# Optimization experiments

Hardware: AMD Instinct MI355X
Metric: run time of the kernel (lower is better)

The kernel has to match this reference:

```python
import jax, jax.numpy as jnp
import numpy as np
from jax import lax

N_GROUPS, TOP_K, CALIB_SCALE = 4, 3, 2.0


def setup_inputs() -> dict:
    key = jax.random.key(0)
    ks = jax.random.split(key, 32)
    d = {}
    d['x'] = jax.random.normal(ks[0], (64, 64, 8192), jnp.float32)
    d['conv_weight'] = jax.random.normal(ks[1], (64, 64, 3), jnp.float32) * 0.05
    d['bias'] = jax.random.normal(ks[2], (64,), jnp.float32) * 0.05
    d['grads'] = jax.random.normal(ks[3], (12288,), jnp.float32) * 0.01
    d['q_ema'] = jax.random.normal(ks[4], (4416,), jnp.float32) * 0.1
    d['ctrl_w'] = jax.random.normal(ks[5], (64, 192), jnp.float32) * 0.07
    d['ctrl_b'] = jnp.zeros((64,), jnp.float32)
    d['gp_w'] = jax.random.normal(ks[6], (64, 65), jnp.float32) * 0.1
    d['gp_b'] = jnp.zeros((64,), jnp.float32)
    d['gt_w'] = jax.random.normal(ks[7], (64, 64), jnp.float32) * 0.1
    d['gt_b'] = jnp.zeros((64,), jnp.float32)
    d['ln_g'] = jnp.ones((64,), jnp.float32)
    d['ln_b'] = jnp.zeros((64,), jnp.float32)
    d['ccin_w'] = jax.random.normal(ks[8], (64, 64), jnp.float32) * 0.05
    d['ccin_b'] = jnp.zeros((64,), jnp.float32)
    d['ck_w'] = jax.random.normal(ks[9], (3, 64), jnp.float32) * 0.05
    d['ck_b'] = jnp.zeros((3,), jnp.float32)
    d['cb_w'] = jax.random.normal(ks[10], (1, 64), jnp.float32) * 0.05
    d['cb_b'] = jnp.zeros((1,), jnp.float32)
    d['cf_w'] = jax.random.normal(ks[11], (1, 64), jnp.float32) * 0.05
    d['cf_b'] = jnp.zeros((1,), jnp.float32)
    d['tau_w'] = jax.random.normal(ks[12], (1, 64), jnp.float32) * 0.1
    d['tau_b'] = jnp.zeros((1,), jnp.float32)
    W = jax.random.normal(ks[13], (4, 1104, 32), jnp.float32)
    d['mem_W'] = W / jnp.linalg.norm(W, axis=1, keepdims=True)  # column-normalized codebook
    d['temp_logit'] = jnp.zeros((4,), jnp.float32)
    return d


def reference(x, conv_weight, bias, grads, q_ema, ctrl_w, ctrl_b, gp_w, gp_b,
              gt_w, gt_b, ln_g, ln_b, ccin_w, ccin_b, ck_w, ck_b, cb_w, cb_b,
              cf_w, cf_b, tau_w, tau_b, mem_W, temp_logit):
    C_out, C_in, K = conv_weight.shape
    cpg = C_out // N_GROUPS
    cin_tot, k_tot = C_out * C_in, C_out * K
    shift = 0.0  # shift_magnitude

    # --- controller: grads -> calibration query q ---
    g = grads.reshape(C_out, C_in * K)
    h = jax.nn.silu(g @ ctrl_w.T + ctrl_b)
    gn = jnp.linalg.norm(g, axis=-1, keepdims=True)
    z = jax.nn.sigmoid(jnp.concatenate([h, gn], -1) @ gp_w.T + gp_b)
    h_t = jax.nn.silu(h @ gt_w.T + gt_b)
    hm = (1.0 - z) * h + z * h_t
    mu = hm.mean(-1, keepdims=True)
    var = ((hm - mu) ** 2).mean(-1, keepdims=True)
    h = ln_g * (hm - mu) / jnp.sqrt(var + 1e-5) + ln_b

    w_cin = jnp.tanh(h @ ccin_w.T + ccin_b) * CALIB_SCALE   # [C_out, C_in]
    w_k = jnp.tanh(h @ ck_w.T + ck_b) * CALIB_SCALE         # [C_out, K]
    b_r = jnp.tanh(h @ cb_w.T + cb_b)[:, 0] * CALIB_SCALE   # [C_out]
    f_r = jnp.tanh(h @ cf_w.T + cf_b)[:, 0] * CALIB_SCALE   # [C_out]
    tau = jax.nn.sigmoid(h @ tau_w.T + tau_b).mean() * 0.5 + 0.5

    q = jnp.concatenate([w_cin.reshape(-1), w_k.reshape(-1), b_r, f_r])
    q = 0.7 * q + 0.3 * lax.stop_gradient(q_ema)

    # --- channel-grouped codebook retrieval (trigger path) ---
    qd = lax.stop_gradient(q)
    q_groups = jnp.concatenate([
        qd[:cin_tot].reshape(N_GROUPS, cpg * C_in),
        qd[cin_tot:cin_tot + k_tot].reshape(N_GROUPS, cpg * K),
        qd[cin_tot + k_tot:cin_tot + k_tot + C_out].reshape(N_GROUPS, cpg),
        qd[cin_tot + k_tot + C_out:].reshape(N_GROUPS, cpg)], axis=1)  # [G, gq]
    temp = (jax.nn.sigmoid(temp_logit) * 0.6 + 0.2) / (1.0 + shift)     # [G]
    att = jnp.einsum('gd,gdm->gm', q_groups, mem_W)
    att = jax.nn.softmax(att / (temp[:, None] + 1e-8), axis=1)
    v, idx = lax.top_k(att, TOP_K)                                      # [G, k]
    gath = jnp.take_along_axis(mem_W, idx[:, None, :], axis=2)          # [G, gq, k]
    retrieved = (gath * v[:, None, :]).sum(-1)                          # [G, gq]

    s0, s1, s2 = cpg * C_in, cpg * (C_in + K), cpg * (C_in + K + 1)
    retrieved_global = jnp.concatenate([
        retrieved[:, :s0].reshape(-1),
        retrieved[:, s0:s1].reshape(-1),
        retrieved[:, s1:s2].reshape(-1),
        retrieved[:, s2:].reshape(-1)])
    q = tau * q + (1.0 - tau) * lax.stop_gradient(retrieved_global)

    # --- split q and modulate conv ---
    w_cin = q[:cin_tot].reshape(C_out, C_in)
    w_k = q[cin_tot:cin_tot + k_tot].reshape(C_out, K)
    b_c = q[cin_tot + k_tot:cin_tot + k_tot + C_out]
    f_c = q[cin_tot + k_tot + C_out:]

    w = conv_weight * (1.0 + w_cin)[:, :, None] * (1.0 + w_k)[:, None, :]
    pad = ((K - 1) * 1 + 1) // 2  # receptive_field // 2 (dilation=1)
    out = lax.conv_general_dilated(x, w, window_strides=(1,),
                                   padding=[(pad, pad)], rhs_dilation=(1,),
                                   dimension_numbers=('NCH', 'OIH', 'NCH'))
    out = out + (bias * (1.0 + b_c))[None, :, None]
    out = out * (1.0 + f_c)[None, :, None]
    return out
```

## Files before the change

kernel.cpp:

```cpp
#include <hip/hip_runtime.h>
#include <math.h>

typedef __attribute__((ext_vector_type(8))) short bf16x8;
typedef __attribute__((ext_vector_type(4))) float f32x4;

__device__ __forceinline__ float sigmoidf_(float x) { return 1.f / (1.f + expf(-x)); }

__device__ __forceinline__ unsigned short f2bf(float f) {
  unsigned int u = __float_as_uint(f);
  u += 0x7fffu + ((u >> 16) & 1u);
  return (unsigned short)(u >> 16);
}
__device__ __forceinline__ float bf2f(unsigned short u) {
  return __uint_as_float(((unsigned int)u) << 16);
}

#define WS_QG    0
#define WS_TAU   4416
#define WS_BEFF  4448
#define WS_SEFF  4512
#define WS_WFRAG 4608

__global__ __launch_bounds__(1024) void kA(
    const float* __restrict__ grads, const float* __restrict__ ctrl_w, const float* __restrict__ ctrl_b,
    const float* __restrict__ gp_w, const float* __restrict__ gp_b,
    const float* __restrict__ gt_w, const float* __restrict__ gt_b,
    const float* __restrict__ ln_g, const float* __restrict__ ln_b,
    const float* __restrict__ ccin_w, const float* __restrict__ ccin_b,
    const float* __restrict__ ck_w, const float* __restrict__ ck_b,
    const float* __restrict__ cb_w, const float* __restrict__ cb_b,
    const float* __restrict__ cf_w, const float* __restrict__ cf_b,
    const float* __restrict__ tau_w, const float* __restrict__ tau_b,
    const float* __restrict__ q_ema, float* __restrict__ ws) {
  __shared__ float rawA[8514];
  __shared__ float sh_h[64 * 65];
  __shared__ float gnp[64 * 17];
  __shared__ float taup[64];
  const int tid = threadIdx.x;
  const int j = tid & 63;
  const int wv = tid >> 6;
  const int i0 = wv * 4;
  const int i0u = __builtin_amdgcn_readfirstlane(i0);

  float acc[4] = {0.f, 0.f, 0.f, 0.f};
  for (int hh = 0; hh < 2; ++hh) {
    const int d0 = hh * 96;
    for (int t = tid; t < 6144; t += 1024) {
      int jj = t / 96, dl = t - jj * 96;
      rawA[dl * 66 + jj] = ctrl_w[jj * 192 + d0 + dl];
    }
    __syncthreads();
    const float* g0 = grads + i0u * 192 + d0;
#pragma unroll 8
    for (int dl = 0; dl < 96; ++dl) {
      float wvv = rawA[dl * 66 + j];
      acc[0] += wvv * g0[dl];
      acc[1] += wvv * g0[192 + dl];
      acc[2] += wvv * g0[384 + dl];
      acc[3] += wvv * g0[576 + dl];
    }
    __syncthreads();
  }
  {
    float cb_ = ctrl_b[j];
#pragma unroll
    for (int ii = 0; ii < 4; ++ii) {
      float s = acc[ii] + cb_;
      sh_h[(i0 + ii) * 65 + j] = s * sigmoidf_(s);
    }
  }
  {
    int gi = tid >> 4, seg = tid & 15;
    const float* gr = grads + gi * 192 + seg * 12;
    float ss = 0.f;
#pragma unroll
    for (int m = 0; m < 12; ++m) { float v = gr[m]; ss += v * v; }
    gnp[gi * 17 + seg] = ss;
  }
  __syncthreads();
  if (tid < 64) {
    float s = 0.f;
#pragma unroll
    for (int seg = 0; seg < 16; ++seg) s += gnp[tid * 17 + seg];
    gnp[tid * 17 + 16] = sqrtf(s);
  }
  for (int t = tid; t < 4096; t += 1024) rawA[(t & 63) * 66 + (t >> 6)] = gt_w[t];
  for (int t = tid; t < 4160; t += 1024) {
    int jj = t / 65, dd = t - jj * 65;
    rawA[4224 + dd * 66 + jj] = gp_w[t];
  }
  __syncthreads();

  float hm[4];
  {
    float zacc[4] = {0.f, 0.f, 0.f, 0.f}, tacc[4] = {0.f, 0.f, 0.f, 0.f};
#pragma unroll 4
    for (int d = 0; d < 64; ++d) {
      float gtv = rawA[d * 66 + j];
      float gpv = rawA[4224 + d * 66 + j];
#pragma unroll
      for (int ii = 0; ii < 4; ++ii) {
        float hv = sh_h[(i0 + ii) * 65 + d];
        tacc[ii] += hv * gtv;
        zacc[ii] += hv * gpv;
      }
    }
    float gplast = rawA[4224 + 64 * 66 + j];
    float zb = gp_b[j], tb = gt_b[j];
#pragma unroll
    for (int ii = 0; ii < 4; ++ii) {
      float gn_ = gnp[(i0 + ii) * 17 + 16];
      float zs = zacc[ii] + gn_ * gplast + zb;
      float ts = tacc[ii] + tb;
      float z = sigmoidf_(zs);
      float ht = ts * sigmoidf_(ts);
      hm[ii] = (1.f - z) * sh_h[(i0 + ii) * 65 + j] + z * ht;
    }
  }
  __syncthreads();
#pragma unroll
  for (int ii = 0; ii < 4; ++ii) sh_h[(i0 + ii) * 65 + j] = hm[ii];
  __syncthreads();

  {
    float lg = ln_g[j], lb = ln_b[j];
#pragma unroll
    for (int ii = 0; ii < 4; ++ii) {
      float x = sh_h[(i0 + ii) * 65 + j];
      float s = x;
#pragma unroll
      for (int off = 32; off; off >>= 1) s += __shfl_xor(s, off);
      float mu = s * (1.f / 64.f);
      float dv = x - mu;
      float v2 = dv * dv;
#pragma unroll
      for (int off = 32; off; off >>= 1) v2 += __shfl_xor(v2, off);
      float invs = 1.f / sqrtf(v2 * (1.f / 64.f) + 1e-5f);
      sh_h[(i0 + ii) * 65 + j] = lg * dv * invs + lb;
    }
  }
  for (int t = tid; t < 4096; t += 1024) rawA[(t & 63) * 66 + (t >> 6)] = ccin_w[t];
  if (tid < 384) {
    int c = tid >> 6, d = tid & 63;
    float v = (c < 3) ? ck_w[c * 64 + d] : (c == 3) ? cb_w[d] : (c == 4) ? cf_w[d] : tau_w[d];
    rawA[4224 + c * 64 + d] = v;
  }
  __syncthreads();

  {
    float cb_ = ccin_b[j];
    float s4[4] = {0.f, 0.f, 0.f, 0.f};
#pragma unroll 4
    for (int d = 0; d < 64; ++d) {
      float cv = rawA[d * 66 + j];
#pragma unroll
      for (int ii = 0; ii < 4; ++ii) s4[ii] += sh_h[(i0 + ii) * 65 + d] * cv;
    }
#pragma unroll
    for (int ii = 0; ii < 4; ++ii) {
      int i = i0 + ii;
      float val = 2.f * tanhf(s4[ii] + cb_);
      ws[WS_QG + (i >> 4) * 1104 + (i & 15) * 64 + j] = 0.7f * val + 0.3f * q_ema[i * 64 + j];
    }
  }
  if (wv < 6) {
    int i = j;
    float s = 0.f;
    const float* er = rawA + 4224 + wv * 64;
#pragma unroll 4
    for (int d = 0; d < 64; ++d) s += sh_h[i * 65 + d] * er[d];
    if (wv < 3) {
      float val = 2.f * tanhf(s + ck_b[wv]);
      ws[WS_QG + (i >> 4) * 1104 + 1024 + (i & 15) * 3 + wv] = 0.7f * val + 0.3f * q_ema[4096 + i * 3 + wv];
    } else if (wv == 3) {
      float val = 2.f * tanhf(s + cb_b[0]);
      ws[WS_QG + (i >> 4) * 1104 + 1072 + (i & 15)] = 0.7f * val + 0.3f * q_ema[4288 + i];
    } else if (wv == 4) {
      float val = 2.f * tanhf(s + cf_b[0]);
      ws[WS_QG + (i >> 4) * 1104 + 1088 + (i & 15)] = 0.7f * val + 0.3f * q_ema[4352 + i];
    } else {
      taup[i] = sigmoidf_(s + tau_b[0]);
    }
  }
  __syncthreads();
  if (tid < 64) {
    float t_ = taup[tid];
#pragma unroll
    for (int off = 32; off; off >>= 1) t_ += __shfl_xor(t_, off);
    if (tid == 0) ws[WS_TAU] = (t_ * (1.f / 64.f)) * 0.5f + 0.5f;
  }
}

__global__ __launch_bounds__(512) void kBD(
    const float* __restrict__ mem_W, const float* __restrict__ temp_logit,
    const float* __restrict__ conv_weight, const float* __restrict__ bias,
    float* __restrict__ ws) {
  __shared__ float qs[1104];
  __shared__ float part[8 * 32];
  __shared__ float sv[3];
  __shared__ int sidx[3];
  __shared__ float qc1[16][64];
  __shared__ float qk1[16][3];
  const int tid = threadIdx.x;
  const int g = blockIdx.x;
  const int wave = tid >> 6, lane = tid & 63;
  const int dl = lane >> 3, m4 = lane & 7;
  for (int t = tid; t < 1104; t += 512) qs[t] = ws[WS_QG + g * 1104 + t];
  __syncthreads();
  const float* mwg = mem_W + (size_t)g * 1104 * 32;
  {
    float4 a = {0.f, 0.f, 0.f, 0.f};
    for (int it = 0; it < 18; ++it) {
      int d = it * 64 + wave * 8 + dl;
      if (d < 1104) {
        float4 v4 = *(const float4*)(mwg + (size_t)d * 32 + m4 * 4);
        float qv = qs[d];
        a.x += qv * v4.x; a.y += qv * v4.y; a.z += qv * v4.z; a.w += qv * v4.w;
      }
    }
#pragma unroll
    for (int off = 8; off <= 32; off <<= 1) {
      a.x += __shfl_xor(a.x, off); a.y += __shfl_xor(a.y, off);
      a.z += __shfl_xor(a.z, off); a.w += __shfl_xor(a.w, off);
    }
    if (dl == 0) {
      float* p = part + wave * 32 + m4 * 4;
      p[0] = a.x; p[1] = a.y; p[2] = a.z; p[3] = a.w;
    }
  }
  __syncthreads();
  if (tid < 32) {
    int m = tid;
    float att = 0.f;
#pragma unroll
    for (int w = 0; w < 8; ++w) att += part[w * 32 + m];
    float temp = 0.6f * sigmoidf_(temp_logit[g]) + 0.2f;
    att /= (temp + 1e-8f);
    float mx = att;
#pragma unroll
    for (int off = 16; off; off >>= 1) mx = fmaxf(mx, __shfl_xor(mx, off, 32));
    float e = expf(att - mx);
    float s = e;
#pragma unroll
    for (int off = 16; off; off >>= 1) s += __shfl_xor(s, off, 32);
    float p = e / s;
    for (int t = 0; t < 3; ++t) {
      float bp = p; int bm = m;
#pragma unroll
      for (int off = 16; off; off >>= 1) {
        float op = __shfl_xor(bp, off, 32);
        int om = __shfl_xor(bm, off, 32);
        if (op > bp || (op == bp && om < bm)) { bp = op; bm = om; }
      }
      if (m == 0) { sv[t] = bp; sidx[t] = bm; }
      if (m == bm) p = -1.f;
    }
  }
  __syncthreads();
  const float tau = ws[WS_TAU];
  const float v0 = sv[0], v1 = sv[1], v2 = sv[2];
  const int x0 = sidx[0], x1 = sidx[1], x2 = sidx[2];
#pragma unroll
  for (int rr = 0; rr < 2; ++rr) {
    int cl = wave + 8 * rr;
    int co = 16 * g + cl;
    {
      int d = cl * 64 + lane;
      float r = v0 * mwg[(size_t)d * 32 + x0] + v1 * mwg[(size_t)d * 32 + x1] + v2 * mwg[(size_t)d * 32 + x2];
      qc1[cl][lane] = 1.f + tau * qs[d] + (1.f - tau) * r;
    }
    if (lane < 3) {
      int d = 1024 + cl * 3 + lane;
      float r = v0 * mwg[(size_t)d * 32 + x0] + v1 * mwg[(size_t)d * 32 + x1] + v2 * mwg[(size_t)d * 32 + x2];
      qk1[cl][lane] = 1.f + tau * qs[d] + (1.f - tau) * r;
    }
    if (lane == 3) {
      int d = 1072 + cl;
      float r = v0 * mwg[(size_t)d * 32 + x0] + v1 * mwg[(size_t)d * 32 + x1] + v2 * mwg[(size_t)d * 32 + x2];
      float qb = tau * qs[d] + (1.f - tau) * r;
      ws[WS_BEFF + co] = bias[co] * (1.f + qb);
    }
    if (lane == 4) {
      int d = 1088 + cl;
      float r = v0 * mwg[(size_t)d * 32 + x0] + v1 * mwg[(size_t)d * 32 + x1] + v2 * mwg[(size_t)d * 32 + x2];
      ws[WS_SEFF + co] = 1.f + tau * qs[d] + (1.f - tau) * r;
    }
  }
  __syncthreads();
  unsigned short* wfrag = (unsigned short*)(ws + WS_WFRAG);
  for (int idx = tid; idx < 3072; idx += 512) {
    int cl = idx / 192, rem = idx - cl * 192;
    int kk = rem >> 6, ci = rem & 63;
    int co = 16 * g + cl;
    float val = conv_weight[(co * 64 + ci) * 3 + kk] * qc1[cl][ci] * qk1[cl][kk];
    int e = kk * 64 + ci;
    int s = e >> 5, hi = (e >> 3) & 3, jj = e & 7;
    wfrag[s * 2048 + g * 512 + (16 * hi + cl) * 8 + jj] = f2bf(val);
  }
}

__global__ __launch_bounds__(256, 4) void k3_y(
    const float* __restrict__ x, const unsigned short* __restrict__ wfrag,
    const float* __restrict__ beff, const float* __restrict__ seff,
    float* __restrict__ out) {
  __shared__ unsigned short xs[128 * 66];
  __shared__ float lhal[64], rhal[64];
  const int tid = threadIdx.x;
  const int w = tid >> 6, l = tid & 63;
  const int g = l >> 4, c16 = l & 15;
  const int n = blockIdx.y;
  const int l0 = blockIdx.x * 128;

  bf16x8 wf[6];
#pragma unroll
  for (int s = 0; s < 6; ++s)
    wf[s] = *(const bf16x8*)(wfrag + s * 2048 + w * 512 + l * 8);

  if (tid < 128) {
    int side = tid >> 6, ci = tid & 63;
    int gp = side ? (l0 + 128) : (l0 - 1);
    float v = (gp >= 0 && gp < 8192) ? x[((size_t)(n * 64 + ci)) * 8192 + gp] : 0.f;
    (side ? rhal : lhal)[ci] = v;
  }

  {
    const float* xb = x + (size_t)n * 64 * 8192 + l0;
#pragma unroll
    for (int s2 = 0; s2 < 2; ++s2) {
      int cp = 8 * w + 4 * s2 + g;
      const float* r0 = xb + (size_t)(2 * cp) * 8192;
      const float* r1 = r0 + 8192;
#pragma unroll
      for (int rep = 0; rep < 2; ++rep) {
        int p = 4 * c16 + 64 * rep;
        float4 va = *(const float4*)(r0 + p);
        float4 vb = *(const float4*)(r1 + p);
        unsigned u0 = (unsigned)f2bf(va.x) | ((unsigned)f2bf(vb.x) << 16);
        unsigned u1 = (unsigned)f2bf(va.y) | ((unsigned)f2bf(vb.y) << 16);
        unsigned u2 = (unsigned)f2bf(va.z) | ((unsigned)f2bf(vb.z) << 16);
        unsigned u3 = (unsigned)f2bf(va.w) | ((unsigned)f2bf(vb.w) << 16);
        *(unsigned*)&xs[(p + 0) * 66 + 2 * cp] = u0;
        *(unsigned*)&xs[(p + 1) * 66 + 2 * cp] = u1;
        *(unsigned*)&xs[(p + 2) * 66 + 2 * cp] = u2;
        *(unsigned*)&xs[(p + 3) * 66 + 2 * cp] = u3;
      }
    }
  }
  __syncthreads();

  float s0 = 0.f, s2s = 0.f;
#pragma unroll
  for (int s = 0; s < 2; ++s) {
#pragma unroll
    for (int jj = 0; jj < 8; ++jj) {
      int ci = 32 * s + 8 * g + jj;
      s0  += bf2f((unsigned short)wf[s][jj]) * lhal[ci];
      s2s += bf2f((unsigned short)wf[4 + s][jj]) * rhal[ci];
    }
  }
  s0 += __shfl_xor(s0, 16);  s0 += __shfl_xor(s0, 32);
  s2s += __shfl_xor(s2s, 16); s2s += __shfl_xor(s2s, 32);
  float carry0 = s0;

  f32x4 o[8];
#pragma unroll
  for (int nt = 0; nt < 8; ++nt) o[nt] = (f32x4){0.f, 0.f, 0.f, 0.f};

#pragma unroll
  for (int nt = 0; nt < 8; ++nt) {
    union { bf16x8 v; unsigned u[4]; } A0, A1;
    const int rbase = (16 * nt + c16) * 66;
#pragma unroll
    for (int k = 0; k < 4; ++k) {
      A0.u[k] = *(const unsigned*)&xs[rbase + 8 * g + 2 * k];
      A1.u[k] = *(const unsigned*)&xs[rbase + 32 + 8 * g + 2 * k];
    }
    o[nt] = __builtin_amdgcn_mfma_f32_16x16x32_bf16(A0.v, wf[2], o[nt], 0, 0, 0);
    o[nt] = __builtin_amdgcn_mfma_f32_16x16x32_bf16(A1.v, wf[3], o[nt], 0, 0, 0);
    f32x4 y0 = (f32x4){0.f, 0.f, 0.f, 0.f};
    f32x4 y2 = (f32x4){0.f, 0.f, 0.f, 0.f};
    y0 = __builtin_amdgcn_mfma_f32_16x16x32_bf16(A0.v, wf[0], y0, 0, 0, 0);
    y0 = __builtin_amdgcn_mfma_f32_16x16x32_bf16(A1.v, wf[1], y0, 0, 0, 0);
    y2 = __builtin_amdgcn_mfma_f32_16x16x32_bf16(A0.v, wf[4], y2, 0, 0, 0);
    y2 = __builtin_amdgcn_mfma_f32_16x16x32_bf16(A1.v, wf[5], y2, 0, 0, 0);
    float sh = __shfl(y0[3], (l - 16) & 63);
    o[nt][0] += (g == 0) ? carry0 : sh;
    o[nt][1] += y0[0];
    o[nt][2] += y0[1];
    o[nt][3] += y0[2];
    carry0 = sh;
    float b0 = __shfl(y2[0], (l + 16) & 63);
    o[nt][0] += y2[1];
    o[nt][1] += y2[2];
    o[nt][2] += y2[3];
    o[nt][3] += (g < 3) ? b0 : 0.f;
    if (nt > 0) o[nt - 1][3] += (g == 3) ? b0 : 0.f;
  }
  o[7][3] += (g == 3) ? s2s : 0.f;

  const int co = 16 * w + c16;
  const float be = beff[co], se = seff[co];
  float* orow = out + ((size_t)(n * 64 + co)) * 8192 + l0 + 4 * g;
#pragma unroll
  for (int nt = 0; nt < 8; ++nt) {
    float4 ov;
    ov.x = se * (o[nt][0] + be);
    ov.y = se * (o[nt][1] + be);
    ov.z = se * (o[nt][2] + be);
    ov.w = se * (o[nt][3] + be);
    *(float4*)(orow + nt * 16) = ov;
  }
}

extern "C" void kernel_launch(void* const* d_in, const int* in_sizes, int n_in,
                              void* d_out, int out_size, void* d_ws, size_t ws_size,
                              hipStream_t stream) {
  const float* x = (const float*)d_in[0];
  const float* conv_weight = (const float*)d_in[1];
  const float* bias = (const float*)d_in[2];
  const float* grads = (const float*)d_in[3];
  const float* q_ema = (const float*)d_in[4];
  const float* ctrl_w = (const float*)d_in[5];
  const float* ctrl_b = (const float*)d_in[6];
  const float* gp_w = (const float*)d_in[7];
  const float* gp_b = (const float*)d_in[8];
  const float* gt_w = (const float*)d_in[9];
  const float* gt_b = (const float*)d_in[10];
  const float* ln_g = (const float*)d_in[11];
  const float* ln_b = (const float*)d_in[12];
  const float* ccin_w = (const float*)d_in[13];
  const float* ccin_b = (const float*)d_in[14];
  const float* ck_w = (const float*)d_in[15];
  const float* ck_b = (const float*)d_in[16];
  const float* cb_w = (const float*)d_in[17];
  const float* cb_b = (const float*)d_in[18];
  const float* cf_w = (const float*)d_in[19];
  const float* cf_b = (const float*)d_in[20];
  const float* tau_w = (const float*)d_in[21];
  const float* tau_b = (const float*)d_in[22];
  const float* mem_W = (const float*)d_in[23];
  const float* temp_logit = (const float*)d_in[24];

  float* ws = (float*)d_ws;

  hipLaunchKernelGGL(kA, dim3(1), dim3(1024), 0, stream,
                     grads, ctrl_w, ctrl_b, gp_w, gp_b, gt_w, gt_b, ln_g, ln_b,
                     ccin_w, ccin_b, ck_w, ck_b, cb_w, cb_b, cf_w, cf_b,
                     tau_w, tau_b, q_ema, ws);
  hipLaunchKernelGGL(kBD, dim3(4), dim3(512), 0, stream, mem_W, temp_logit, conv_weight, bias, ws);
  hipLaunchKernelGGL(k3_y, dim3(64, 64), dim3(256), 0, stream,
                     x, (const unsigned short*)(ws + WS_WFRAG), ws + WS_BEFF, ws + WS_SEFF,
                     (float*)d_out);
}
```

Baseline: 123.1 us.

## Fuse controller and retrieval kernels, widen conv tile, swizzle LDS layout

Merges the single-block controller kernel and the 4-block retrieval kernel into one 4-block launch. Each block recomputes the controller redundantly and keeps q and tau in shared memory instead of passing them through global workspace, which removes one launch. The conv kernel now processes 256 positions per block instead of 128, and its shared-memory x tile uses an XOR swizzle in place of padding, with 64-bit LDS reads. Trade-offs are the repeated controller work, more accumulator registers (16 f32x4), and half as many conv blocks, which may lower occupancy.

Measured after the change: 205.4 us. +66.8%, slower.

```diff
diff --git a/kernel.cpp b/kernel.cpp
--- a/kernel.cpp
+++ b/kernel.cpp
@@ -3,6 +3,7 @@
 
 typedef __attribute__((ext_vector_type(8))) short bf16x8;
 typedef __attribute__((ext_vector_type(4))) float f32x4;
+typedef unsigned long long ull;
 
 __device__ __forceinline__ float sigmoidf_(float x) { return 1.f / (1.f + expf(-x)); }
 
@@ -15,13 +16,11 @@
   return __uint_as_float(((unsigned int)u) << 16);
 }
 
-#define WS_QG    0
-#define WS_TAU   4416
-#define WS_BEFF  4448
-#define WS_SEFF  4512
-#define WS_WFRAG 4608
-
-__global__ __launch_bounds__(1024) void kA(
+#define WS_BEFF  0
+#define WS_SEFF  64
+#define WS_WFRAG 128
+
+__global__ __launch_bounds__(1024) void kCtl(
     const float* __restrict__ grads, const float* __restrict__ ctrl_w, const float* __restrict__ ctrl_b,
     const float* __restrict__ gp_w, const float* __restrict__ gp_b,
     const float* __restrict__ gt_w, const float* __restrict__ gt_b,
@@ -31,12 +30,23 @@
     const float* __restrict__ cb_w, const float* __restrict__ cb_b,
     const float* __restrict__ cf_w, const float* __restrict__ cf_b,
     const float* __restrict__ tau_w, const float* __restrict__ tau_b,
-    const float* __restrict__ q_ema, float* __restrict__ ws) {
+    const float* __restrict__ q_ema, const float* __restrict__ mem_W,
+    const float* __restrict__ temp_logit,
+    const float* __restrict__ conv_weight, const float* __restrict__ bias,
+    float* __restrict__ ws) {
   __shared__ float rawA[8514];
   __shared__ float sh_h[64 * 65];
   __shared__ float gnp[64 * 17];
   __shared__ float taup[64];
+  __shared__ float sh_qg[4416];
+  __shared__ float part[16][32];
+  __shared__ float sv[3];
+  __shared__ int sidx[3];
+  __shared__ float qc1[16][64];
+  __shared__ float qk1[16][3];
+  __shared__ float sh_tau;
   const int tid = threadIdx.x;
+  const int g = blockIdx.x;
   const int j = tid & 63;
   const int wv = tid >> 6;
   const int i0 = wv * 4;
@@ -160,7 +170,7 @@
     for (int ii = 0; ii < 4; ++ii) {
       int i = i0 + ii;
       float val = 2.f * tanhf(s4[ii] + cb_);
-      ws[WS_QG + (i >> 4) * 1104 + (i & 15) * 64 + j] = 0.7f * val + 0.3f * q_ema[i * 64 + j];
+      sh_qg[(i >> 4) * 1104 + (i & 15) * 64 + j] = 0.7f * val + 0.3f * q_ema[i * 64 + j];
     }
   }
   if (wv < 6) {
@@ -171,13 +181,13 @@
     for (int d = 0; d < 64; ++d) s += sh_h[i * 65 + d] * er[d];
     if (wv < 3) {
       float val = 2.f * tanhf(s + ck_b[wv]);
-      ws[WS_QG + (i >> 4) * 1104 + 1024 + (i & 15) * 3 + wv] = 0.7f * val + 0.3f * q_ema[4096 + i * 3 + wv];
+      sh_qg[(i >> 4) * 1104 + 1024 + (i & 15) * 3 + wv] = 0.7f * val + 0.3f * q_ema[4096 + i * 3 + wv];
     } else if (wv == 3) {
       float val = 2.f * tanhf(s + cb_b[0]);
-      ws[WS_QG + (i >> 4) * 1104 + 1072 + (i & 15)] = 0.7f * val + 0.3f * q_ema[4288 + i];
+      sh_qg[(i >> 4) * 1104 + 1072 + (i & 15)] = 0.7f * val + 0.3f * q_ema[4288 + i];
     } else if (wv == 4) {
       float val = 2.f * tanhf(s + cf_b[0]);
-      ws[WS_QG + (i >> 4) * 1104 + 1088 + (i & 15)] = 0.7f * val + 0.3f * q_ema[4352 + i];
+      sh_qg[(i >> 4) * 1104 + 1088 + (i & 15)] = 0.7f * val + 0.3f * q_ema[4352 + i];
     } else {
       taup[i] = sigmoidf_(s + tau_b[0]);
     }
@@ -187,34 +197,20 @@
     float t_ = taup[tid];
 #pragma unroll
     for (int off = 32; off; off >>= 1) t_ += __shfl_xor(t_, off);
-    if (tid == 0) ws[WS_TAU] = (t_ * (1.f / 64.f)) * 0.5f + 0.5f;
-  }
-}
-
-__global__ __launch_bounds__(512) void kBD(
-    const float* __restrict__ mem_W, const float* __restrict__ temp_logit,
-    const float* __restrict__ conv_weight, const float* __restrict__ bias,
-    float* __restrict__ ws) {
-  __shared__ float qs[1104];
-  __shared__ float part[8 * 32];
-  __shared__ float sv[3];
-  __shared__ int sidx[3];
-  __shared__ float qc1[16][64];
-  __shared__ float qk1[16][3];
-  const int tid = threadIdx.x;
-  const int g = blockIdx.x;
-  const int wave = tid >> 6, lane = tid & 63;
-  const int dl = lane >> 3, m4 = lane & 7;
-  for (int t = tid; t < 1104; t += 512) qs[t] = ws[WS_QG + g * 1104 + t];
-  __syncthreads();
+    if (tid == 0) sh_tau = (t_ * (1.f / 64.f)) * 0.5f + 0.5f;
+  }
+  __syncthreads();
+
   const float* mwg = mem_W + (size_t)g * 1104 * 32;
   {
     float4 a = {0.f, 0.f, 0.f, 0.f};
-    for (int it = 0; it < 18; ++it) {
-      int d = it * 64 + wave * 8 + dl;
+    const float* qg = sh_qg + g * 1104;
+#pragma unroll
+    for (int it = 0; it < 9; ++it) {
+      int d = it * 128 + (tid >> 3);
       if (d < 1104) {
-        float4 v4 = *(const float4*)(mwg + (size_t)d * 32 + m4 * 4);
-        float qv = qs[d];
+        float4 v4 = *(const float4*)(mwg + (size_t)d * 32 + (tid & 7) * 4);
+        float qv = qg[d];
         a.x += qv * v4.x; a.y += qv * v4.y; a.z += qv * v4.z; a.w += qv * v4.w;
       }
     }
@@ -223,17 +219,15 @@
       a.x += __shfl_xor(a.x, off); a.y += __shfl_xor(a.y, off);
       a.z += __shfl_xor(a.z, off); a.w += __shfl_xor(a.w, off);
     }
-    if (dl == 0) {
-      float* p = part + wave * 32 + m4 * 4;
-      p[0] = a.x; p[1] = a.y; p[2] = a.z; p[3] = a.w;
-    }
-  }
-  __syncthreads();
+    if ((tid & 63) < 8) *(float4*)&part[tid >> 6][(tid & 7) * 4] = a;
+  }
+  __syncthreads();
+
   if (tid < 32) {
     int m = tid;
     float att = 0.f;
 #pragma unroll
-    for (int w = 0; w < 8; ++w) att += part[w * 32 + m];
+    for (int w = 0; w < 16; ++w) att += part[w][m];
     float temp = 0.6f * sigmoidf_(temp_logit[g]) + 0.2f;
     att /= (temp + 1e-8f);
     float mx = att;
@@ -257,38 +251,41 @@
     }
   }
   __syncthreads();
-  const float tau = ws[WS_TAU];
-  const float v0 = sv[0], v1 = sv[1], v2 = sv[2];
-  const int x0 = sidx[0], x1 = sidx[1], x2 = sidx[2];
-#pragma unroll
-  for (int rr = 0; rr < 2; ++rr) {
-    int cl = wave + 8 * rr;
+
+  {
+    const float tau = sh_tau;
+    const float v0 = sv[0], v1 = sv[1], v2 = sv[2];
+    const int x0 = sidx[0], x1 = sidx[1], x2 = sidx[2];
+    const float* qg = sh_qg + g * 1104;
+    int cl = wv;
     int co = 16 * g + cl;
+    int lane = j;
     {
       int d = cl * 64 + lane;
       float r = v0 * mwg[(size_t)d * 32 + x0] + v1 * mwg[(size_t)d * 32 + x1] + v2 * mwg[(size_t)d * 32 + x2];
-      qc1[cl][lane] = 1.f + tau * qs[d] + (1.f - tau) * r;
+      qc1[cl][lane] = 1.f + tau * qg[d] + (1.f - tau) * r;
     }
     if (lane < 3) {
       int d = 1024 + cl * 3 + lane;
       float r = v0 * mwg[(size_t)d * 32 + x0] + v1 * mwg[(size_t)d * 32 + x1] + v2 * mwg[(size_t)d * 32 + x2];
-      qk1[cl][lane] = 1.f + tau * qs[d] + (1.f - tau) * r;
+      qk1[cl][lane] = 1.f + tau * qg[d] + (1.f - tau) * r;
     }
     if (lane == 3) {
       int d = 1072 + cl;
       float r = v0 * mwg[(size_t)d * 32 + x0] + v1 * mwg[(size_t)d * 32 + x1] + v2 * mwg[(size_t)d * 32 + x2];
-      float qb = tau * qs[d] + (1.f - tau) * r;
+      float qb = tau * qg[d] + (1.f - tau) * r;
       ws[WS_BEFF + co] = bias[co] * (1.f + qb);
     }
     if (lane == 4) {
       int d = 1088 + cl;
       float r = v0 * mwg[(size_t)d * 32 + x0] + v1 * mwg[(size_t)d * 32 + x1] + v2 * mwg[(size_t)d * 32 + x2];
-      ws[WS_SEFF + co] = 1.f + tau * qs[d] + (1.f - tau) * r;
-    }
-  }
-  __syncthreads();
+      ws[WS_SEFF + co] = 1.f + tau * qg[d] + (1.f - tau) * r;
+    }
+  }
+  __syncthreads();
+
   unsigned short* wfrag = (unsigned short*)(ws + WS_WFRAG);
-  for (int idx = tid; idx < 3072; idx += 512) {
+  for (int idx = tid; idx < 3072; idx += 1024) {
     int cl = idx / 192, rem = idx - cl * 192;
     int kk = rem >> 6, ci = rem & 63;
     int co = 16 * g + cl;
@@ -303,46 +300,42 @@
     const float* __restrict__ x, const unsigned short* __restrict__ wfrag,
     const float* __restrict__ beff, const float* __restrict__ seff,
     float* __restrict__ out) {
-  __shared__ unsigned short xs[128 * 66];
+  __shared__ unsigned short xs[256 * 64];
   __shared__ float lhal[64], rhal[64];
   const int tid = threadIdx.x;
   const int w = tid >> 6, l = tid & 63;
   const int g = l >> 4, c16 = l & 15;
   const int n = blockIdx.y;
-  const int l0 = blockIdx.x * 128;
+  const int l0 = blockIdx.x * 256;
 
   bf16x8 wf[6];
 #pragma unroll
   for (int s = 0; s < 6; ++s)
     wf[s] = *(const bf16x8*)(wfrag + s * 2048 + w * 512 + l * 8);
 
-  if (tid < 128) {
-    int side = tid >> 6, ci = tid & 63;
-    int gp = side ? (l0 + 128) : (l0 - 1);
-    float v = (gp >= 0 && gp < 8192) ? x[((size_t)(n * 64 + ci)) * 8192 + gp] : 0.f;
-    (side ? rhal : lhal)[ci] = v;
-  }
-
-  {
-    const float* xb = x + (size_t)n * 64 * 8192 + l0;
-#pragma unroll
-    for (int s2 = 0; s2 < 2; ++s2) {
-      int cp = 8 * w + 4 * s2 + g;
-      const float* r0 = xb + (size_t)(2 * cp) * 8192;
-      const float* r1 = r0 + 8192;
-#pragma unroll
-      for (int rep = 0; rep < 2; ++rep) {
-        int p = 4 * c16 + 64 * rep;
-        float4 va = *(const float4*)(r0 + p);
-        float4 vb = *(const float4*)(r1 + p);
-        unsigned u0 = (unsigned)f2bf(va.x) | ((unsigned)f2bf(vb.x) << 16);
-        unsigned u1 = (unsigned)f2bf(va.y) | ((unsigned)f2bf(vb.y) << 16);
-        unsigned u2 = (unsigned)f2bf(va.z) | ((unsigned)f2bf(vb.z) << 16);
-        unsigned u3 = (unsigned)f2bf(va.w) | ((unsigned)f2bf(vb.w) << 16);
-        *(unsigned*)&xs[(p + 0) * 66 + 2 * cp] = u0;
-        *(unsigned*)&xs[(p + 1) * 66 + 2 * cp] = u1;
-        *(unsigned*)&xs[(p + 2) * 66 + 2 * cp] = u2;
-        *(unsigned*)&xs[(p + 3) * 66 + 2 * cp] = u3;
+  if (tid < 64) {
+    const float* rowp = x + ((size_t)(n * 64 + tid)) * 8192;
+    lhal[tid] = (l0 > 0) ? rowp[l0 - 1] : 0.f;
+    rhal[tid] = (l0 + 256 < 8192) ? rowp[l0 + 256] : 0.f;
+  }
+
+  {
+    const int cp = 8 * w + (l >> 3);
+    const float* r0 = x + ((size_t)(n * 64 + 2 * cp)) * 8192 + l0;
+    const float* r1 = r0 + 8192;
+    char* xb = (char*)xs;
+#pragma unroll
+    for (int t = 0; t < 8; ++t) {
+      int p0 = 4 * ((l & 7) + 8 * t);
+      float4 va = *(const float4*)(r0 + p0);
+      float4 vb = *(const float4*)(r1 + p0);
+      float av[4] = {va.x, va.y, va.z, va.w};
+      float bv[4] = {vb.x, vb.y, vb.z, vb.w};
+#pragma unroll
+      for (int i = 0; i < 4; ++i) {
+        int pos = p0 + i;
+        unsigned u = (unsigned)f2bf(av[i]) | ((unsigned)f2bf(bv[i]) << 16);
+        *(unsigned*)(xb + pos * 128 + ((4 * cp) ^ ((pos & 15) << 3))) = u;
       }
     }
   }
@@ -362,19 +355,20 @@
   s2s += __shfl_xor(s2s, 16); s2s += __shfl_xor(s2s, 32);
   float carry0 = s0;
 
-  f32x4 o[8];
-#pragma unroll
-  for (int nt = 0; nt < 8; ++nt) o[nt] = (f32x4){0.f, 0.f, 0.f, 0.f};
-
-#pragma unroll
-  for (int nt = 0; nt < 8; ++nt) {
-    union { bf16x8 v; unsigned u[4]; } A0, A1;
-    const int rbase = (16 * nt + c16) * 66;
-#pragma unroll
-    for (int k = 0; k < 4; ++k) {
-      A0.u[k] = *(const unsigned*)&xs[rbase + 8 * g + 2 * k];
-      A1.u[k] = *(const unsigned*)&xs[rbase + 32 + 8 * g + 2 * k];
-    }
+  f32x4 o[16];
+#pragma unroll
+  for (int nt = 0; nt < 16; ++nt) o[nt] = (f32x4){0.f, 0.f, 0.f, 0.f};
+
+  const char* xbc = (const char*)xs;
+  const int sw = c16 << 3;
+#pragma unroll
+  for (int nt = 0; nt < 16; ++nt) {
+    const int rbase = (16 * nt + c16) * 128;
+    union { bf16x8 v; ull d[2]; } A0, A1;
+    A0.d[0] = *(const ull*)(xbc + rbase + ((16 * g) ^ sw));
+    A0.d[1] = *(const ull*)(xbc + rbase + ((16 * g + 8) ^ sw));
+    A1.d[0] = *(const ull*)(xbc + rbase + ((64 + 16 * g) ^ sw));
+    A1.d[1] = *(const ull*)(xbc + rbase + ((64 + 16 * g + 8) ^ sw));
     o[nt] = __builtin_amdgcn_mfma_f32_16x16x32_bf16(A0.v, wf[2], o[nt], 0, 0, 0);
     o[nt] = __builtin_amdgcn_mfma_f32_16x16x32_bf16(A1.v, wf[3], o[nt], 0, 0, 0);
     f32x4 y0 = (f32x4){0.f, 0.f, 0.f, 0.f};
@@ -396,13 +390,13 @@
     o[nt][3] += (g < 3) ? b0 : 0.f;
     if (nt > 0) o[nt - 1][3] += (g == 3) ? b0 : 0.f;
   }
-  o[7][3] += (g == 3) ? s2s : 0.f;
+  o[15][3] += (g == 3) ? s2s : 0.f;
 
   const int co = 16 * w + c16;
   const float be = beff[co], se = seff[co];
   float* orow = out + ((size_t)(n * 64 + co)) * 8192 + l0 + 4 * g;
 #pragma unroll
-  for (int nt = 0; nt < 8; ++nt) {
+  for (int nt = 0; nt < 16; ++nt) {
     float4 ov;
     ov.x = se * (o[nt][0] + be);
     ov.y = se * (o[nt][1] + be);
@@ -443,12 +437,11 @@
 
   float* ws = (float*)d_ws;
 
-  hipLaunchKernelGGL(kA, dim3(1), dim3(1024), 0, stream,
+  hipLaunchKernelGGL(kCtl, dim3(4), dim3(1024), 0, stream,
                      grads, ctrl_w, ctrl_b, gp_w, gp_b, gt_w, gt_b, ln_g, ln_b,
                      ccin_w, ccin_b, ck_w, ck_b, cb_w, cb_b, cf_w, cf_b,
-                     tau_w, tau_b, q_ema, ws);
-  hipLaunchKernelGGL(kBD, dim3(4), dim3(512), 0, stream, mem_W, temp_logit, conv_weight, bias, ws);
-  hipLaunchKernelGGL(k3_y, dim3(64, 64), dim3(256), 0, stream,
+                     tau_w, tau_b, q_ema, mem_W, temp_logit, conv_weight, bias, ws);
+  hipLaunchKernelGGL(k3_y, dim3(32, 64), dim3(256), 0, stream,
                      x, (const unsigned short*)(ws + WS_WFRAG), ws + WS_BEFF, ws + WS_SEFF,
                      (float*)d_out);
 }
```
